# Kernel optimization log

Hardware: AMD Instinct MI355X
Metric: run time of the kernel (lower is better)

Reference implementation:

```python
import jax, jax.numpy as jnp
import numpy as np

B, INDIM, OUTDIM = 4096, 640, 64
EPS = 1e-6


def setup_inputs() -> dict:
    key = jax.random.key(0)
    k1, k2 = jax.random.split(key)
    x = jax.random.normal(k1, (B, INDIM), dtype=jnp.float32)
    # weight_v of nn.Linear(indim, outdim): shape [outdim, indim]
    weight_v = jax.random.normal(k2, (OUTDIM, INDIM), dtype=jnp.float32) / np.sqrt(INDIM)
    # temp initialized to zeros(1) - 1
    temp = jnp.full((1,), -1.0, dtype=jnp.float32)
    return {"x": x, "weight_v": weight_v, "temp": temp}


def reference(x, weight_v, temp):
    # x: [B, indim]; weight_v: [outdim, indim]; temp: [1]
    # L2-normalize rows of (x + eps), exactly as torch.norm(x + 1e-6, dim=1)
    xn = x / jnp.linalg.norm(x + EPS, axis=1, keepdims=True)  # [B, indim]
    outdim, indim = weight_v.shape
    # Faithful to torch: transpose THEN row-major reshape (scrambles layout
    # unless indim == outdim).
    w = weight_v.T.reshape(1, outdim, indim)  # [1, outdim, indim]
    diff = xn[:, None, :] - w                 # [B, outdim, indim] (large intermediate)
    dist = jnp.sqrt(jnp.sum(diff * diff, axis=2))  # [B, outdim]
    return temp * dist
```

## Files before the change

### kernel.cpp

```cpp
#include <hip/hip_runtime.h>
#include <math.h>

#define EPSV 1e-6f

typedef short bf16x8 __attribute__((ext_vector_type(8)));
typedef float f32x4 __attribute__((ext_vector_type(4)));

static __device__ __forceinline__ short f2bf(float f) {
    unsigned u = __builtin_bit_cast(unsigned, f);
    unsigned r = u + 0x7FFFu + ((u >> 16) & 1u);
    return (short)(r >> 16);
}
static __device__ __forceinline__ float bf2f(short s) {
    return __builtin_bit_cast(float, ((unsigned)(unsigned short)s) << 16);
}

__global__ __launch_bounds__(1024) void fused_all(
    const float* __restrict__ x, const float* __restrict__ wv,
    const float* __restrict__ temp, float* __restrict__ out) {
    __shared__ __align__(16) short wf[40960];
    __shared__ f32x4 ldsacc[3][4][64];
    __shared__ float2 ldsn[4][16];
    __shared__ float ldsnw[4][4][16];

    const int tid = threadIdx.x;

    {
        const int t15 = tid & 15;
        const int r = tid >> 4;
        const float4* wrow = (const float4*)wv + tid * 10;
        char* wfb = (char*)wf + (r >> 5) * 4096
                    + (t15 >> 2) * 1024
                    + ((t15 & 3) * 4) * 16
                    + (((r >> 3) & 3)) * 256
                    + (r & 7) * 2;
#pragma unroll
        for (int q = 0; q < 10; ++q) {
            float4 v = wrow[q];
            float vals[4] = {v.x, v.y, v.z, v.w};
#pragma unroll
            for (int e2 = 0; e2 < 4; ++e2) {
                const int m = q * 4 + e2;
                const int md = m / 10;
                const int mm = m % 10;
                *(short*)(wfb + mm * 8192 + md * 16) = f2bf(vals[e2]);
            }
        }
    }
    __syncthreads();

    const int l = tid & 63, lm = l & 15, lg = l >> 4;
    const int w = tid >> 6;
    const int ct = w & 3, kseg = w >> 2;
    const int rt = blockIdx.x;

    const float* xr = x + (rt * 16 + lm) * 640 + kseg * 160 + lg * 8;
    const bf16x8* wfq = (const bf16x8*)wf;
    const int qb = ((kseg * 5) * 4 + ct) * 64 + l;

    f32x4 acc = {0.f, 0.f, 0.f, 0.f};
    float s2 = 0.f, sv = 0.f, nw = 0.f;
#pragma unroll
    for (int s = 0; s < 5; ++s) {
        float4 a0 = *(const float4*)(xr + s * 32);
        float4 a1 = *(const float4*)(xr + s * 32 + 4);
        bf16x8 b = wfq[qb + s * 256];
        bf16x8 a;
        a[0] = f2bf(a0.x); a[1] = f2bf(a0.y); a[2] = f2bf(a0.z); a[3] = f2bf(a0.w);
        a[4] = f2bf(a1.x); a[5] = f2bf(a1.y); a[6] = f2bf(a1.z); a[7] = f2bf(a1.w);
        s2 += a0.x * a0.x + a0.y * a0.y + a0.z * a0.z + a0.w * a0.w
            + a1.x * a1.x + a1.y * a1.y + a1.z * a1.z + a1.w * a1.w;
        sv += (a0.x + a0.y + a0.z + a0.w) + (a1.x + a1.y + a1.z + a1.w);
#pragma unroll
        for (int e = 0; e < 8; ++e) { float bw = bf2f(b[e]); nw += bw * bw; }
        acc = __builtin_amdgcn_mfma_f32_16x16x32_bf16(a, b, acc, 0, 0, 0);
    }

    s2 += __shfl_xor(s2, 16); s2 += __shfl_xor(s2, 32);
    sv += __shfl_xor(sv, 16); sv += __shfl_xor(sv, 32);
    nw += __shfl_xor(nw, 16); nw += __shfl_xor(nw, 32);
    if (lg == 0) {
        ldsnw[kseg][ct][lm] = nw;
        if (ct == 0) ldsn[kseg][lm] = make_float2(s2, sv);
    }
    if (kseg > 0) ldsacc[kseg - 1][ct][l] = acc;
    __syncthreads();

    if (kseg == 0) {
#pragma unroll
        for (int p = 0; p < 3; ++p) {
            f32x4 t = ldsacc[p][ct][l];
            acc[0] += t[0]; acc[1] += t[1]; acc[2] += t[2]; acc[3] += t[3];
        }
        float nwv = ldsnw[0][ct][lm] + ldsnw[1][ct][lm] +
                    ldsnw[2][ct][lm] + ldsnw[3][ct][lm];
        float tv = temp[0];
#pragma unroll
        for (int i = 0; i < 4; ++i) {
            int rr = lg * 4 + i;
            float2 n0 = ldsn[0][rr], n1 = ldsn[1][rr];
            float2 n2 = ldsn[2][rr], n3 = ldsn[3][rr];
            float S2 = n0.x + n1.x + n2.x + n3.x;
            float SV = n0.y + n1.y + n2.y + n3.y;
            float S1 = S2 + 2.f * EPSV * SV + 640.f * EPSV * EPSV;
            float iv = rsqrtf(S1);
            float nx = S2 * iv * iv;
            float d2 = nx - 2.f * acc[i] * iv + nwv;
            out[(rt * 16 + rr) * 64 + ct * 16 + lm] = tv * sqrtf(fmaxf(d2, 0.f));
        }
    }
}

extern "C" void kernel_launch(void* const* d_in, const int* in_sizes, int n_in,
                              void* d_out, int out_size, void* d_ws, size_t ws_size,
                              hipStream_t stream) {
    const float* x = (const float*)d_in[0];
    const float* wv = (const float*)d_in[1];
    const float* temp = (const float*)d_in[2];
    float* out = (float*)d_out;

    fused_all<<<256, 1024, 0, stream>>>(x, wv, temp, out);
}
```

Baseline: 16.80 us.

## Compute norms via MFMA, hardware bf16 packing, prefetch x before weight staging

Row norms of x and column norms of W are now taken from diagonals of extra MFMAs (A·A and B·B) rather than scalar FMA loops and shuffles. Conversion to bf16 uses the packed v_cvt_pk_bf16_f32 instruction, and the weight staging is reorganized so each thread writes packed 32-bit pairs. The x loads are issued before the weight staging so they overlap with it. The eps correction is dropped and ||xn||^2 is assumed to be 1, and the x norm now comes from bf16-rounded values, which changes numerics slightly.

```diff
diff --git a/kernel.cpp b/kernel.cpp
--- a/kernel.cpp
+++ b/kernel.cpp
@@ -1,18 +1,13 @@
 #include <hip/hip_runtime.h>
 #include <math.h>
-
-#define EPSV 1e-6f
 
 typedef short bf16x8 __attribute__((ext_vector_type(8)));
 typedef float f32x4 __attribute__((ext_vector_type(4)));
 
-static __device__ __forceinline__ short f2bf(float f) {
-    unsigned u = __builtin_bit_cast(unsigned, f);
-    unsigned r = u + 0x7FFFu + ((u >> 16) & 1u);
-    return (short)(r >> 16);
-}
-static __device__ __forceinline__ float bf2f(short s) {
-    return __builtin_bit_cast(float, ((unsigned)(unsigned short)s) << 16);
+static __device__ __forceinline__ unsigned cvt_pk_bf16(float lo, float hi) {
+    unsigned r;
+    asm("v_cvt_pk_bf16_f32 %0, %1, %2" : "=v"(r) : "v"(lo), "v"(hi));
+    return r;
 }
 
 __global__ __launch_bounds__(1024) void fused_all(
@@ -20,68 +15,66 @@
     const float* __restrict__ temp, float* __restrict__ out) {
     __shared__ __align__(16) short wf[40960];
     __shared__ f32x4 ldsacc[3][4][64];
-    __shared__ float2 ldsn[4][16];
+    __shared__ float ldsn[4][16];
     __shared__ float ldsnw[4][4][16];
 
     const int tid = threadIdx.x;
-
-    {
-        const int t15 = tid & 15;
-        const int r = tid >> 4;
-        const float4* wrow = (const float4*)wv + tid * 10;
-        char* wfb = (char*)wf + (r >> 5) * 4096
-                    + (t15 >> 2) * 1024
-                    + ((t15 & 3) * 4) * 16
-                    + (((r >> 3) & 3)) * 256
-                    + (r & 7) * 2;
-#pragma unroll
-        for (int q = 0; q < 10; ++q) {
-            float4 v = wrow[q];
-            float vals[4] = {v.x, v.y, v.z, v.w};
-#pragma unroll
-            for (int e2 = 0; e2 < 4; ++e2) {
-                const int m = q * 4 + e2;
-                const int md = m / 10;
-                const int mm = m % 10;
-                *(short*)(wfb + mm * 8192 + md * 16) = f2bf(vals[e2]);
-            }
-        }
-    }
-    __syncthreads();
-
     const int l = tid & 63, lm = l & 15, lg = l >> 4;
     const int w = tid >> 6;
     const int ct = w & 3, kseg = w >> 2;
     const int rt = blockIdx.x;
 
     const float* xr = x + (rt * 16 + lm) * 640 + kseg * 160 + lg * 8;
-    const bf16x8* wfq = (const bf16x8*)wf;
-    const int qb = ((kseg * 5) * 4 + ct) * 64 + l;
-
-    f32x4 acc = {0.f, 0.f, 0.f, 0.f};
-    float s2 = 0.f, sv = 0.f, nw = 0.f;
+    float4 xa[10];
 #pragma unroll
     for (int s = 0; s < 5; ++s) {
-        float4 a0 = *(const float4*)(xr + s * 32);
-        float4 a1 = *(const float4*)(xr + s * 32 + 4);
+        xa[2 * s]     = *(const float4*)(xr + s * 32);
+        xa[2 * s + 1] = *(const float4*)(xr + s * 32 + 4);
+    }
+    float tv = temp[0];
+
+#pragma unroll
+    for (int it = 0; it < 2; ++it) {
+        const int cg = (tid & 7) | (((tid >> 5) & 7) << 3);
+        const int rp = ((tid >> 3) & 3) | (((tid >> 8) & 3) << 2) | (it << 4);
+        const float* r0 = wv + (2 * rp) * 640 + 10 * cg;
+        const float* r1 = r0 + 640;
+        char* base = (char*)wf + (rp >> 4) * 4096 + (cg >> 4) * 1024 +
+                     (cg & 15) * 16 + ((rp >> 2) & 3) * 256 + 4 * (rp & 3);
+#pragma unroll
+        for (int j = 0; j < 5; ++j) {
+            float2 va = *(const float2*)(r0 + 2 * j);
+            float2 vb = *(const float2*)(r1 + 2 * j);
+            *(unsigned*)(base + (2 * j) * 8192)     = cvt_pk_bf16(va.x, vb.x);
+            *(unsigned*)(base + (2 * j + 1) * 8192) = cvt_pk_bf16(va.y, vb.y);
+        }
+    }
+    __syncthreads();
+
+    const bf16x8* wfq = (const bf16x8*)wf;
+    const int qb = (kseg * 20 + ct) * 64 + l;
+
+    f32x4 acc  = {0.f, 0.f, 0.f, 0.f};
+    f32x4 accW = {0.f, 0.f, 0.f, 0.f};
+    f32x4 accG = {0.f, 0.f, 0.f, 0.f};
+#pragma unroll
+    for (int s = 0; s < 5; ++s) {
         bf16x8 b = wfq[qb + s * 256];
-        bf16x8 a;
-        a[0] = f2bf(a0.x); a[1] = f2bf(a0.y); a[2] = f2bf(a0.z); a[3] = f2bf(a0.w);
-        a[4] = f2bf(a1.x); a[5] = f2bf(a1.y); a[6] = f2bf(a1.z); a[7] = f2bf(a1.w);
-        s2 += a0.x * a0.x + a0.y * a0.y + a0.z * a0.z + a0.w * a0.w
-            + a1.x * a1.x + a1.y * a1.y + a1.z * a1.z + a1.w * a1.w;
-        sv += (a0.x + a0.y + a0.z + a0.w) + (a1.x + a1.y + a1.z + a1.w);
-#pragma unroll
-        for (int e = 0; e < 8; ++e) { float bw = bf2f(b[e]); nw += bw * bw; }
-        acc = __builtin_amdgcn_mfma_f32_16x16x32_bf16(a, b, acc, 0, 0, 0);
+        float4 a0 = xa[2 * s], a1 = xa[2 * s + 1];
+        union { unsigned u[4]; bf16x8 v; } A;
+        A.u[0] = cvt_pk_bf16(a0.x, a0.y);
+        A.u[1] = cvt_pk_bf16(a0.z, a0.w);
+        A.u[2] = cvt_pk_bf16(a1.x, a1.y);
+        A.u[3] = cvt_pk_bf16(a1.z, a1.w);
+        acc  = __builtin_amdgcn_mfma_f32_16x16x32_bf16(A.v, b, acc, 0, 0, 0);
+        accW = __builtin_amdgcn_mfma_f32_16x16x32_bf16(b, b, accW, 0, 0, 0);
+        if (ct == 0)
+            accG = __builtin_amdgcn_mfma_f32_16x16x32_bf16(A.v, A.v, accG, 0, 0, 0);
     }
 
-    s2 += __shfl_xor(s2, 16); s2 += __shfl_xor(s2, 32);
-    sv += __shfl_xor(sv, 16); sv += __shfl_xor(sv, 32);
-    nw += __shfl_xor(nw, 16); nw += __shfl_xor(nw, 32);
-    if (lg == 0) {
-        ldsnw[kseg][ct][lm] = nw;
-        if (ct == 0) ldsn[kseg][lm] = make_float2(s2, sv);
+    if ((lm >> 2) == lg) {
+        ldsnw[kseg][ct][lm] = accW[lm & 3];
+        if (ct == 0) ldsn[kseg][lm] = accG[lm & 3];
     }
     if (kseg > 0) ldsacc[kseg - 1][ct][l] = acc;
     __syncthreads();
@@ -89,23 +82,17 @@
     if (kseg == 0) {
 #pragma unroll
         for (int p = 0; p < 3; ++p) {
-            f32x4 t = ldsacc[p][ct][l];
-            acc[0] += t[0]; acc[1] += t[1]; acc[2] += t[2]; acc[3] += t[3];
+            f32x4 t2 = ldsacc[p][ct][l];
+            acc[0] += t2[0]; acc[1] += t2[1]; acc[2] += t2[2]; acc[3] += t2[3];
         }
         float nwv = ldsnw[0][ct][lm] + ldsnw[1][ct][lm] +
                     ldsnw[2][ct][lm] + ldsnw[3][ct][lm];
-        float tv = temp[0];
 #pragma unroll
         for (int i = 0; i < 4; ++i) {
             int rr = lg * 4 + i;
-            float2 n0 = ldsn[0][rr], n1 = ldsn[1][rr];
-            float2 n2 = ldsn[2][rr], n3 = ldsn[3][rr];
-            float S2 = n0.x + n1.x + n2.x + n3.x;
-            float SV = n0.y + n1.y + n2.y + n3.y;
-            float S1 = S2 + 2.f * EPSV * SV + 640.f * EPSV * EPSV;
-            float iv = rsqrtf(S1);
-            float nx = S2 * iv * iv;
-            float d2 = nx - 2.f * acc[i] * iv + nwv;
+            float S2 = ldsn[0][rr] + ldsn[1][rr] + ldsn[2][rr] + ldsn[3][rr];
+            float iv = rsqrtf(S2);
+            float d2 = 1.0f - 2.f * acc[i] * iv + nwv;
             out[(rt * 16 + rr) * 64 + ct * 16 + lm] = tv * sqrtf(fmaxf(d2, 0.f));
         }
     }
```

Result: faster. 14.20 us (-15.5%).
